# Kernel tuning notes

Measured on AMD Instinct MI355X. Metric: run time of the kernel, lower is better.

Reference implementation:

```python
import jax, jax.numpy as jnp
import numpy as np

EPS = 1e-5

def layer_norm(x, w, b):
    mu = jnp.mean(x, axis=-1, keepdims=True)
    var = jnp.mean(jnp.square(x - mu), axis=-1, keepdims=True)
    return (x - mu) * jax.lax.rsqrt(var + EPS) * w + b

def setup_inputs() -> dict:
    key = jax.random.key(0)
    ks = jax.random.split(key, 8)
    B, T, C = 8, 512, 768
    s = 1.0 / np.sqrt(C)
    s4 = 1.0 / np.sqrt(4 * C)
    return {
        "x": jax.random.normal(ks[0], (B, T, C), dtype=jnp.float32),
        "ln1_w": jnp.ones((C,), jnp.float32),
        "ln1_b": jnp.zeros((C,), jnp.float32),
        "Wr": jax.random.normal(ks[1], (C, C), dtype=jnp.float32) * s,
        "Wk": jax.random.normal(ks[2], (C, C), dtype=jnp.float32) * s,
        "Wv": jax.random.normal(ks[3], (C, C), dtype=jnp.float32) * s,
        "time_mix_w": jnp.ones((C,), jnp.float32),  # torch init: torch.ones(n_embd)
        "Wrouter": jax.random.normal(ks[4], (C, C), dtype=jnp.float32) * s,
        "ln2_w": jnp.ones((C,), jnp.float32),
        "ln2_b": jnp.zeros((C,), jnp.float32),
        "Wck": jax.random.normal(ks[5], (4 * C, C), dtype=jnp.float32) * s,
        "Wcv": jax.random.normal(ks[6], (C, 4 * C), dtype=jnp.float32) * s4,
    }

def reference(x, ln1_w, ln1_b, Wr, Wk, Wv, time_mix_w, Wrouter, ln2_w, ln2_b, Wck, Wcv):
    B, T, C = x.shape
    xx = layer_norm(x, ln1_w, ln1_b)
    r = xx @ Wr.T
    k = xx @ Wk.T
    v = xx @ Wv.T
    w = -jnp.exp(time_mix_w)                        # (C,) negative per-channel decay rate
    idx = jnp.arange(T)
    diff = jnp.clip(idx[:, None] - idx[None, :], 0).astype(x.dtype)  # (T,T) t-j clamped at 0
    causal = jnp.tril(jnp.ones((T, T), x.dtype))
    decay = jnp.exp(w[:, None, None] * diff[None]) * causal          # (C,T,T)
    kv = k * v                                                       # (B,T,C)
    # wkv[b,t,c] = sum_j decay[c,t,j] * kv[b,j,c]
    wkv = jnp.einsum('ctj,bjc->btc', decay, kv)
    routed_wkv = wkv * jax.nn.sigmoid(xx @ Wrouter.T)
    x = x + r * routed_wkv
    xx2 = layer_norm(x, ln2_w, ln2_b)
    k_cm = jnp.square(jax.nn.relu(xx2 @ Wck.T))                      # (B,T,4C)
    return x + k_cm @ Wcv.T
```

## Files before the change

kernel.cpp:

```cpp
#include <hip/hip_runtime.h>
#include <hip/hip_bf16.h>

typedef __bf16 bf16_t;
typedef __bf16 bf16x8 __attribute__((ext_vector_type(8)));
typedef __bf16 bf16x4 __attribute__((ext_vector_type(4)));
typedef __bf16 bf16x2 __attribute__((ext_vector_type(2)));
typedef float  f32x4  __attribute__((ext_vector_type(4)));

#define LN_EPS 1e-5f


typedef __attribute__((address_space(1))) void gvoid_t;
typedef __attribute__((address_space(3))) void lvoid_t;
__device__ __forceinline__ void glds16(const void* g, void* l) {
    __builtin_amdgcn_global_load_lds((gvoid_t*)g, (lvoid_t*)l, 16, 0, 0);
}

__global__ __launch_bounds__(256) void k_cvt4(const float* __restrict__ s0,
                                              const float* __restrict__ s1,
                                              const float* __restrict__ s2,
                                              const float* __restrict__ s3,
                                              bf16_t* __restrict__ dst, int n4) {
    const float* s = (blockIdx.y == 0) ? s0 : (blockIdx.y == 1) ? s1 : (blockIdx.y == 2) ? s2 : s3;
    bf16_t* d = dst + (size_t)blockIdx.y * ((size_t)n4 * 4);
    int i = blockIdx.x * 256 + threadIdx.x;
    if (i < n4) {
        float4 v = ((const float4*)s)[i];
        bf16x4 o;
        o.x = (bf16_t)v.x; o.y = (bf16_t)v.y; o.z = (bf16_t)v.z; o.w = (bf16_t)v.w;
        ((bf16x4*)d)[i] = o;
    }
}

__global__ __launch_bounds__(256) void k_cvt2(const float* __restrict__ s0,
                                              const float* __restrict__ s1,
                                              bf16_t* __restrict__ dst, int n4) {
    const float* s = (blockIdx.y == 0) ? s0 : s1;
    bf16_t* d = dst + (size_t)blockIdx.y * ((size_t)n4 * 4);
    int i = blockIdx.x * 256 + threadIdx.x;
    if (i < n4) {
        float4 v = ((const float4*)s)[i];
        bf16x4 o;
        o.x = (bf16_t)v.x; o.y = (bf16_t)v.y; o.z = (bf16_t)v.z; o.w = (bf16_t)v.w;
        ((bf16x4*)d)[i] = o;
    }
}

__global__ __launch_bounds__(256) void k_ln(const float* __restrict__ x,
                                            const float* __restrict__ w,
                                            const float* __restrict__ b,
                                            bf16_t* __restrict__ out, int C) {
    int row = blockIdx.x;
    const float* xr = x + (long)row * C;
    int tid = threadIdx.x;
    float s = 0.f, s2 = 0.f;
    for (int i = tid; i < C; i += 256) { float v = xr[i]; s += v; s2 += v * v; }
    for (int m = 32; m; m >>= 1) { s += __shfl_xor(s, m, 64); s2 += __shfl_xor(s2, m, 64); }
    __shared__ float red[8];
    int wv = tid >> 6;
    if ((tid & 63) == 0) { red[wv] = s; red[4 + wv] = s2; }
    __syncthreads();
    float ts  = red[0] + red[1] + red[2] + red[3];
    float ts2 = red[4] + red[5] + red[6] + red[7];
    float mu  = ts / C;
    float var = ts2 / C - mu * mu;
    float rstd = rsqrtf(var + LN_EPS);
    bf16_t* orow = out + (long)row * C;
    for (int i = tid; i < C; i += 256)
        orow[i] = (bf16_t)((xr[i] - mu) * rstd * w[i] + b[i]);
}

template <int EPI>
__global__ __launch_bounds__(512, 2) void k_gemm_bt(const bf16_t* __restrict__ A,
                                                    const bf16_t* __restrict__ Bw,
                                                    void* __restrict__ Cout,
                                                    int N, int Ktot, int nbn, int nks) {
    constexpr int TBUF = 256 * 64;
    __shared__ __align__(16) bf16_t As[2][256][64];
    __shared__ __align__(16) bf16_t Bs[2][256][64];
    const int tid  = threadIdx.x;
    const int lane = tid & 63, wid = tid >> 6;
    const int wm = (wid >> 2) * 128, wn = (wid & 3) * 64;

    int bid = blockIdx.x;
    int xcd = bid & 7, loc = bid >> 3;
    int bm  = (xcd >> 1) * 4 + loc / 6;
    int cix = (xcd & 1) * 6 + loc % 6;
    int ks  = cix / nbn;
    int bn  = cix % nbn;

    const int fr  = lane & 15;
    const int oct = lane >> 4;
    const int ph0 = ((oct)     ^ (fr & 7)) * 8;
    const int ph1 = ((oct + 4) ^ (fr & 7)) * 8;

    f32x4 acc[8][4];
#pragma unroll
    for (int i = 0; i < 8; i++)
#pragma unroll
        for (int j = 0; j < 4; j++) acc[i][j] = (f32x4){0.f, 0.f, 0.f, 0.f};

    const int srow = wid * 32 + (lane >> 3);
    const int scol = ((lane & 7) ^ (lane >> 3)) * 8;
    const size_t ksoff = (size_t)ks * 768;
    const bf16_t* Ag = A  + (size_t)(bm * 256 + srow) * Ktot + ksoff + scol;
    const bf16_t* Bg = Bw + (size_t)(bn * 256 + srow) * Ktot + ksoff + scol;
    const size_t Kt8 = (size_t)8 * Ktot;
    bf16_t* lA = &As[0][0][0] + (size_t)(wid * 32) * 64;
    bf16_t* lB = &Bs[0][0][0] + (size_t)(wid * 32) * 64;

#define STAGE(buf, kt)                                                     \
    do {                                                                   \
        const bf16_t* a0 = Ag + (size_t)(kt) * 64;                         \
        const bf16_t* b0 = Bg + (size_t)(kt) * 64;                         \
        _Pragma("unroll")                                                  \
        for (int q = 0; q < 4; q++) {                                      \
            glds16(a0 + q * Kt8, lA + (buf) * TBUF + q * 512);             \
            glds16(b0 + q * Kt8, lB + (buf) * TBUF + q * 512);             \
        }                                                                  \
    } while (0)

#define COMPUTE_KK(buf, PH, KOFF)                                                            \
    do {                                                                                     \
        const bf16_t* bA = &As[0][0][0] + (buf) * TBUF;                                      \
        const bf16_t* bB = &Bs[0][0][0] + (buf) * TBUF;                                      \
        bf16x8 bfr[4], af[8];                                                                \
        _Pragma("unroll")                                                                    \
        for (int ni = 0; ni < 4; ni++)                                                       \
            bfr[ni] = *(const bf16x8*)(bB + (wn + ni * 16 + fr) * 64 + (PH));                \
        _Pragma("unroll")                                                                    \
        for (int mi = 0; mi < 8; mi++)                                                       \
            af[mi] = *(const bf16x8*)(bA + (wm + mi * 16 + fr) * 64 + (PH));                 \
        __builtin_amdgcn_s_setprio(1);                                                       \
        _Pragma("unroll")                                                                    \
        for (int mi = 0; mi < 8; mi++)                                                       \
            _Pragma("unroll")                                                                \
            for (int ni = 0; ni < 4; ni++)                                                   \
                acc[mi][ni] = __builtin_amdgcn_mfma_f32_16x16x32_bf16(af[mi], bfr[ni], acc[mi][ni], 0, 0, 0); \
        __builtin_amdgcn_s_setprio(0);                                                       \
    } while (0)

    STAGE(0, 0);
    for (int t = 0; t < 12; ++t) {
        asm volatile("s_waitcnt vmcnt(0)" ::: "memory");
        __builtin_amdgcn_s_barrier();
        __builtin_amdgcn_sched_barrier(0);
        if (t < 11) STAGE((t + 1) & 1, t + 1);
        __builtin_amdgcn_sched_barrier(0);
        COMPUTE_KK(t & 1, ph0, 0);
        COMPUTE_KK(t & 1, ph1, 32);
    }

#undef STAGE
#undef COMPUTE_KK

    const int row0 = bm * 256 + wm, col0 = bn * 256 + wn;
#pragma unroll
    for (int mi = 0; mi < 8; mi++) {
#pragma unroll
        for (int ni = 0; ni < 4; ni++) {
            int row = row0 + mi * 16 + (lane >> 4) * 4;
            int col = col0 + ni * 16 + (lane & 15);
#pragma unroll
            for (int r = 0; r < 4; r++) {
                float val = acc[mi][ni][r];
                size_t off = (size_t)(row + r) * N + col;
                if (EPI == 0) {
                    ((bf16_t*)Cout)[off] = (bf16_t)val;
                } else if (EPI == 1) {
                    float t = fmaxf(val, 0.f);
                    ((bf16_t*)Cout)[off] = (bf16_t)(t * t);
                } else {
                    atomicAdd(&((float*)Cout)[off], val);
                }
            }
        }
    }
}

__global__ __launch_bounds__(256) void k_scan_local(const bf16_t* __restrict__ y4,
                                                    const float* __restrict__ tmw,
                                                    float* __restrict__ wkvl,
                                                    float* __restrict__ states) {
    int idx = blockIdx.x * 256 + threadIdx.x;
    int cp  = idx % 384;
    int rem = idx / 384;
    int ch  = rem & 15;
    int b   = rem >> 4;
    int c   = cp * 2;
    float d0 = expf(-expf(tmw[c]));
    float d1 = expf(-expf(tmw[c + 1]));
    const bf16_t* base = y4 + ((size_t)(b * 512 + ch * 32)) * 3072 + c;
    float*        wout = wkvl + ((size_t)(b * 512 + ch * 32)) * 768 + c;
    float s0 = 0.f, s1 = 0.f;
#pragma unroll 4
    for (int i = 0; i < 32; i++) {
        bf16x2 k2 = *(const bf16x2*)(base + (size_t)i * 3072 + 768);
        bf16x2 v2 = *(const bf16x2*)(base + (size_t)i * 3072 + 1536);
        s0 = s0 * d0 + (float)k2.x * (float)v2.x;
        s1 = s1 * d1 + (float)k2.y * (float)v2.y;
        *(float2*)(wout + (size_t)i * 768) = make_float2(s0, s1);
    }
    *(float2*)(states + ((size_t)(b * 16 + ch)) * 768 + c) = make_float2(s0, s1);
}

__global__ __launch_bounds__(256) void k_scan_carry(const float* __restrict__ states,
                                                    const float* __restrict__ tmw,
                                                    float* __restrict__ carries) {
    int idx = blockIdx.x * 256 + threadIdx.x;
    int c = idx % 768, b = idx / 768;
    float dL = expf(-expf(tmw[c]) * 32.f);
    float s = 0.f;
    for (int ch = 0; ch < 16; ch++) {
        size_t o = ((size_t)(b * 16 + ch)) * 768 + c;
        carries[o] = s;
        s = s * dL + states[o];
    }
}

__global__ __launch_bounds__(256) void k_mix_ln(const bf16_t* __restrict__ y4,
                                                const float* __restrict__ wkvl,
                                                const float* __restrict__ carries,
                                                const float* __restrict__ tmw,
                                                const float* __restrict__ x,
                                                const float* __restrict__ w2,
                                                const float* __restrict__ b2,
                                                float* __restrict__ out,
                                                bf16_t* __restrict__ xx2) {
    int bt = blockIdx.x;
    int t = bt & 511, b = bt >> 9;
    int tid = threadIdx.x;
    const bf16_t* yrow = y4 + (size_t)bt * 3072;
    const float*  wl   = wkvl + (size_t)bt * 768;
    const float*  cr   = carries + ((size_t)(b * 16) + (t >> 5)) * 768;
    const float*  xr   = x + (size_t)bt * 768;
    float tn = (float)((t & 31) + 1);

    float vals[3];
    float s = 0.f, s2 = 0.f;
#pragma unroll
    for (int j = 0; j < 3; j++) {
        int c = tid + j * 256;
        float rr = (float)yrow[c];
        float gg = (float)yrow[c + 2304];
        float wk = wl[c] + cr[c] * expf(-expf(tmw[c]) * tn);
        float sig = 1.f / (1.f + expf(-gg));
        float o = fmaf(rr, wk * sig, xr[c]);
        vals[j] = o; s += o; s2 += o * o;
    }
    for (int m = 32; m; m >>= 1) { s += __shfl_xor(s, m, 64); s2 += __shfl_xor(s2, m, 64); }
    __shared__ float red[8];
    int wv = tid >> 6;
    if ((tid & 63) == 0) { red[wv] = s; red[4 + wv] = s2; }
    __syncthreads();
    float ts  = red[0] + red[1] + red[2] + red[3];
    float ts2 = red[4] + red[5] + red[6] + red[7];
    float mu  = ts * (1.f / 768.f);
    float var = ts2 * (1.f / 768.f) - mu * mu;
    float rstd = rsqrtf(var + LN_EPS);
    float* orow = out + (size_t)bt * 768;
    bf16_t* xo = xx2 + (size_t)bt * 768;
#pragma unroll
    for (int j = 0; j < 3; j++) {
        int c = tid + j * 256;
        orow[c] = vals[j];
        xo[c] = (bf16_t)((vals[j] - mu) * rstd * w2[c] + b2[c]);
    }
}

extern "C" void kernel_launch(void* const* d_in, const int* in_sizes, int n_in,
                              void* d_out, int out_size, void* d_ws, size_t ws_size,
                              hipStream_t stream) {
    const float* x    = (const float*)d_in[0];
    const float* ln1w = (const float*)d_in[1];
    const float* ln1b = (const float*)d_in[2];
    const float* Wr   = (const float*)d_in[3];
    const float* Wk   = (const float*)d_in[4];
    const float* Wv   = (const float*)d_in[5];
    const float* tmw  = (const float*)d_in[6];
    const float* Wrt  = (const float*)d_in[7];
    const float* ln2w = (const float*)d_in[8];
    const float* ln2b = (const float*)d_in[9];
    const float* Wck  = (const float*)d_in[10];
    const float* Wcv  = (const float*)d_in[11];
    float* out = (float*)d_out;
    char* ws = (char*)d_ws;

    bf16_t* xx     = (bf16_t*)(ws + 0);
    bf16_t* wcat   = (bf16_t*)(ws + 6291456);
    bf16_t* wckb   = (bf16_t*)(ws + 11010048);
    bf16_t* wcvb   = (bf16_t*)(ws + 15728640);
    bf16_t* y4     = (bf16_t*)(ws + 20447232);
    bf16_t* kcm    = (bf16_t*)(ws + 20447232);
    float*  wkvl   = (float*)(ws + 70778880);
    float*  states = (float*)(ws + 83361792);
    float*  carr   = (float*)(ws + 83755008);

    const int n768 = 768 * 768 / 4;
    const int nbig = 3072 * 768 / 4;
    k_cvt4<<<dim3(576, 4), dim3(256), 0, stream>>>(Wr, Wk, Wv, Wrt, wcat, n768);
    k_cvt2<<<dim3(2304, 2), dim3(256), 0, stream>>>(Wck, Wcv, wckb, nbig);

    k_ln<<<dim3(4096), dim3(256), 0, stream>>>(x, ln1w, ln1b, xx, 768);

    k_gemm_bt<0><<<dim3(192), dim3(512), 0, stream>>>(xx, wcat, (void*)y4, 3072, 768, 12, 1);

    k_scan_local<<<dim3(192), dim3(256), 0, stream>>>(y4, tmw, wkvl, states);
    k_scan_carry<<<dim3(24), dim3(256), 0, stream>>>(states, tmw, carr);
    k_mix_ln<<<dim3(4096), dim3(256), 0, stream>>>(y4, wkvl, carr, tmw, x, ln2w, ln2b, out, xx);

    k_gemm_bt<1><<<dim3(192), dim3(512), 0, stream>>>(xx, wckb, (void*)kcm, 3072, 768, 12, 1);

    k_gemm_bt<3><<<dim3(192), dim3(512), 0, stream>>>(kcm, wcvb, (void*)out, 768, 3072, 3, 4);
}
```

Before: 164.4 us.

## Replace GEMM with 256x128-tile, triple-buffered, phase-interleaved pipelined kernel

The bf16 GEMM kernel now uses 256x128 output tiles instead of 256x256, doubling the grid to 384 blocks. It triple-buffers LDS so loads run two k-steps ahead. The k-step is split into four phases, each issuing part of the next global-to-LDS copy before its MFMAs, so memory traffic overlaps compute instead of stalling at one barrier per step. This adds extra barriers and lgkmcnt waits per phase, and launch bounds drop to one block per SIMD.

```diff
diff --git a/kernel.cpp b/kernel.cpp
--- a/kernel.cpp
+++ b/kernel.cpp
@@ -71,96 +71,112 @@
 }
 
 template <int EPI>
-__global__ __launch_bounds__(512, 2) void k_gemm_bt(const bf16_t* __restrict__ A,
+__global__ __launch_bounds__(512, 1) void k_gemm_p8(const bf16_t* __restrict__ A,
                                                     const bf16_t* __restrict__ Bw,
                                                     void* __restrict__ Cout,
                                                     int N, int Ktot, int nbn, int nks) {
-    constexpr int TBUF = 256 * 64;
-    __shared__ __align__(16) bf16_t As[2][256][64];
-    __shared__ __align__(16) bf16_t Bs[2][256][64];
+    __shared__ __align__(16) bf16_t As[3][256][64];
+    __shared__ __align__(16) bf16_t Bs[3][128][64];
     const int tid  = threadIdx.x;
     const int lane = tid & 63, wid = tid >> 6;
-    const int wm = (wid >> 2) * 128, wn = (wid & 3) * 64;
+    const int wm = (wid >> 1) * 64, wn = (wid & 1) * 64;
 
     int bid = blockIdx.x;
     int xcd = bid & 7, loc = bid >> 3;
-    int bm  = (xcd >> 1) * 4 + loc / 6;
-    int cix = (xcd & 1) * 6 + loc % 6;
-    int ks  = cix / nbn;
-    int bn  = cix % nbn;
-
-    const int fr  = lane & 15;
-    const int oct = lane >> 4;
-    const int ph0 = ((oct)     ^ (fr & 7)) * 8;
-    const int ph1 = ((oct + 4) ^ (fr & 7)) * 8;
-
-    f32x4 acc[8][4];
-#pragma unroll
-    for (int i = 0; i < 8; i++)
+    int bm  = (xcd & 3) * 4 + loc / 12;
+    int cix = (xcd >> 2) * 12 + loc % 12;
+    int ks  = cix / nbn, bn = cix % nbn;
+
+    const int fr  = lane & 15, oct = lane >> 4;
+    const int f8  = fr & 7;
+    const int ph0 = ((oct)     ^ f8) * 8;
+    const int ph1 = ((oct + 4) ^ f8) * 8;
+
+    f32x4 acc[4][4];
+#pragma unroll
+    for (int i = 0; i < 4; i++)
 #pragma unroll
         for (int j = 0; j < 4; j++) acc[i][j] = (f32x4){0.f, 0.f, 0.f, 0.f};
 
-    const int srow = wid * 32 + (lane >> 3);
-    const int scol = ((lane & 7) ^ (lane >> 3)) * 8;
+    const int sr   = lane >> 3;
+    const int scol = ((lane & 7) ^ sr) * 8;
     const size_t ksoff = (size_t)ks * 768;
-    const bf16_t* Ag = A  + (size_t)(bm * 256 + srow) * Ktot + ksoff + scol;
-    const bf16_t* Bg = Bw + (size_t)(bn * 256 + srow) * Ktot + ksoff + scol;
+    const bf16_t* AgS = A  + (size_t)(bm * 256 + wid * 32 + sr) * Ktot + ksoff + scol;
+    const bf16_t* BgS = Bw + (size_t)(bn * 128 + wid * 16 + sr) * Ktot + ksoff + scol;
     const size_t Kt8 = (size_t)8 * Ktot;
-    bf16_t* lA = &As[0][0][0] + (size_t)(wid * 32) * 64;
-    bf16_t* lB = &Bs[0][0][0] + (size_t)(wid * 32) * 64;
-
-#define STAGE(buf, kt)                                                     \
-    do {                                                                   \
-        const bf16_t* a0 = Ag + (size_t)(kt) * 64;                         \
-        const bf16_t* b0 = Bg + (size_t)(kt) * 64;                         \
-        _Pragma("unroll")                                                  \
-        for (int q = 0; q < 4; q++) {                                      \
-            glds16(a0 + q * Kt8, lA + (buf) * TBUF + q * 512);             \
-            glds16(b0 + q * Kt8, lB + (buf) * TBUF + q * 512);             \
-        }                                                                  \
-    } while (0)
-
-#define COMPUTE_KK(buf, PH, KOFF)                                                            \
+
+#define AGLDS(pr, tt, q) glds16(AgS + (size_t)(tt) * 64 + (q) * Kt8, &As[pr][wid * 32 + (q) * 8][0])
+#define BGLDS(pr, tt, q) glds16(BgS + (size_t)(tt) * 64 + (q) * Kt8, &Bs[pr][wid * 16 + (q) * 8][0])
+
+#define PHASE(P, par, st, pr2, tt2)                                                          \
     do {                                                                                     \
-        const bf16_t* bA = &As[0][0][0] + (buf) * TBUF;                                      \
-        const bf16_t* bB = &Bs[0][0][0] + (buf) * TBUF;                                      \
-        bf16x8 bfr[4], af[8];                                                                \
+        bf16x8 afr[2][2], bfr2[2][2];                                                        \
         _Pragma("unroll")                                                                    \
-        for (int ni = 0; ni < 4; ni++)                                                       \
-            bfr[ni] = *(const bf16x8*)(bB + (wn + ni * 16 + fr) * 64 + (PH));                \
+        for (int m2 = 0; m2 < 2; ++m2) {                                                     \
+            afr[m2][0] = *(const bf16x8*)&As[par][wm + ((P >> 1) * 2 + m2) * 16 + fr][ph0];  \
+            afr[m2][1] = *(const bf16x8*)&As[par][wm + ((P >> 1) * 2 + m2) * 16 + fr][ph1];  \
+        }                                                                                    \
         _Pragma("unroll")                                                                    \
-        for (int mi = 0; mi < 8; mi++)                                                       \
-            af[mi] = *(const bf16x8*)(bA + (wm + mi * 16 + fr) * 64 + (PH));                 \
+        for (int n2 = 0; n2 < 2; ++n2) {                                                     \
+            bfr2[n2][0] = *(const bf16x8*)&Bs[par][wn + ((P & 1) * 2 + n2) * 16 + fr][ph0];  \
+            bfr2[n2][1] = *(const bf16x8*)&Bs[par][wn + ((P & 1) * 2 + n2) * 16 + fr][ph1];  \
+        }                                                                                    \
+        if (st) {                                                                            \
+            if ((P) == 0) { AGLDS(pr2, tt2, 0); AGLDS(pr2, tt2, 1); }                        \
+            if ((P) == 1) { AGLDS(pr2, tt2, 2); AGLDS(pr2, tt2, 3); }                        \
+            if ((P) == 2) { BGLDS(pr2, tt2, 0); }                                            \
+            if ((P) == 3) { BGLDS(pr2, tt2, 1); }                                            \
+        }                                                                                    \
+        asm volatile("s_waitcnt lgkmcnt(0)" ::: "memory");                                   \
+        __builtin_amdgcn_sched_barrier(0);                                                   \
         __builtin_amdgcn_s_setprio(1);                                                       \
         _Pragma("unroll")                                                                    \
-        for (int mi = 0; mi < 8; mi++)                                                       \
+        for (int kk = 0; kk < 2; ++kk)                                                       \
             _Pragma("unroll")                                                                \
-            for (int ni = 0; ni < 4; ni++)                                                   \
-                acc[mi][ni] = __builtin_amdgcn_mfma_f32_16x16x32_bf16(af[mi], bfr[ni], acc[mi][ni], 0, 0, 0); \
+            for (int m2 = 0; m2 < 2; ++m2)                                                   \
+                _Pragma("unroll")                                                            \
+                for (int n2 = 0; n2 < 2; ++n2)                                               \
+                    acc[(P >> 1) * 2 + m2][(P & 1) * 2 + n2] =                               \
+                        __builtin_amdgcn_mfma_f32_16x16x32_bf16(                             \
+                            afr[m2][kk], bfr2[n2][kk],                                       \
+                            acc[(P >> 1) * 2 + m2][(P & 1) * 2 + n2], 0, 0, 0);              \
         __builtin_amdgcn_s_setprio(0);                                                       \
+        __builtin_amdgcn_s_barrier();                                                        \
+        __builtin_amdgcn_sched_barrier(0);                                                   \
     } while (0)
 
-    STAGE(0, 0);
+    AGLDS(0, 0, 0); AGLDS(0, 0, 1); AGLDS(0, 0, 2); AGLDS(0, 0, 3);
+    BGLDS(0, 0, 0); BGLDS(0, 0, 1);
+    AGLDS(1, 1, 0); AGLDS(1, 1, 1); AGLDS(1, 1, 2); AGLDS(1, 1, 3);
+    BGLDS(1, 1, 0); BGLDS(1, 1, 1);
+
+    int par = 0, pr2 = 2;
     for (int t = 0; t < 12; ++t) {
-        asm volatile("s_waitcnt vmcnt(0)" ::: "memory");
+        if (t < 11) { asm volatile("s_waitcnt vmcnt(6)" ::: "memory"); }
+        else        { asm volatile("s_waitcnt vmcnt(0)" ::: "memory"); }
         __builtin_amdgcn_s_barrier();
         __builtin_amdgcn_sched_barrier(0);
-        if (t < 11) STAGE((t + 1) & 1, t + 1);
-        __builtin_amdgcn_sched_barrier(0);
-        COMPUTE_KK(t & 1, ph0, 0);
-        COMPUTE_KK(t & 1, ph1, 32);
-    }
-
-#undef STAGE
-#undef COMPUTE_KK
-
-    const int row0 = bm * 256 + wm, col0 = bn * 256 + wn;
-#pragma unroll
-    for (int mi = 0; mi < 8; mi++) {
+        const bool st  = (t < 10);
+        const int  tt2 = t + 2;
+        PHASE(0, par, st, pr2, tt2);
+        PHASE(1, par, st, pr2, tt2);
+        PHASE(2, par, st, pr2, tt2);
+        PHASE(3, par, st, pr2, tt2);
+        par = (par == 2) ? 0 : par + 1;
+        pr2 = (pr2 == 2) ? 0 : pr2 + 1;
+    }
+
+#undef PHASE
+#undef AGLDS
+#undef BGLDS
+
+    const int row0 = bm * 256 + wm, col0 = bn * 128 + wn;
+#pragma unroll
+    for (int mi = 0; mi < 4; mi++) {
 #pragma unroll
         for (int ni = 0; ni < 4; ni++) {
-            int row = row0 + mi * 16 + (lane >> 4) * 4;
-            int col = col0 + ni * 16 + (lane & 15);
+            int row = row0 + mi * 16 + oct * 4;
+            int col = col0 + ni * 16 + fr;
 #pragma unroll
             for (int r = 0; r < 4; r++) {
                 float val = acc[mi][ni][r];
@@ -303,13 +319,13 @@
 
     k_ln<<<dim3(4096), dim3(256), 0, stream>>>(x, ln1w, ln1b, xx, 768);
 
-    k_gemm_bt<0><<<dim3(192), dim3(512), 0, stream>>>(xx, wcat, (void*)y4, 3072, 768, 12, 1);
+    k_gemm_p8<0><<<dim3(384), dim3(512), 0, stream>>>(xx, wcat, (void*)y4, 3072, 768, 24, 1);
 
     k_scan_local<<<dim3(192), dim3(256), 0, stream>>>(y4, tmw, wkvl, states);
     k_scan_carry<<<dim3(24), dim3(256), 0, stream>>>(states, tmw, carr);
     k_mix_ln<<<dim3(4096), dim3(256), 0, stream>>>(y4, wkvl, carr, tmw, x, ln2w, ln2b, out, xx);
 
-    k_gemm_bt<1><<<dim3(192), dim3(512), 0, stream>>>(xx, wckb, (void*)kcm, 3072, 768, 12, 1);
-
-    k_gemm_bt<3><<<dim3(192), dim3(512), 0, stream>>>(kcm, wcvb, (void*)out, 768, 3072, 3, 4);
-}
+    k_gemm_p8<1><<<dim3(384), dim3(512), 0, stream>>>(xx, wckb, (void*)kcm, 3072, 768, 24, 1);
+
+    k_gemm_p8<3><<<dim3(384), dim3(512), 0, stream>>>(kcm, wcvb, (void*)out, 768, 3072, 6, 4);
+}
```

New measurement: 191.0 us. 16.2% more time.
